# Kernel tuning notes

Hardware: AMD Instinct MI355X
Metric: run time of the kernel (lower is better)

Reference implementation:

```python
import jax, jax.numpy as jnp
import numpy as np

IN, H, OUT, B = 1024, 4096, 1, 4096


def setup_inputs() -> dict:
    key = jax.random.key(0)
    ks = jax.random.split(key, 20)
    sx = 1.0 / np.sqrt(IN)
    sh = 1.0 / np.sqrt(H)
    d = {
        "x": jax.random.normal(ks[0], (B, IN), jnp.float32),
        "hidden": jax.random.normal(ks[1], (B, H), jnp.float32),
        "cell": jax.random.normal(ks[2], (B, H), jnp.float32),
        # input projections (Linear(input_size, h_size)), weight [H, IN], bias [H]
        "Wx_i": jax.random.normal(ks[3], (H, IN), jnp.float32) * sx,
        "Wx_f": jax.random.normal(ks[4], (H, IN), jnp.float32) * sx,
        "Wx_o": jax.random.normal(ks[5], (H, IN), jnp.float32) * sx,
        "Wx_c": jax.random.normal(ks[6], (H, IN), jnp.float32) * sx,
        "bx_i": jax.random.normal(ks[7], (H,), jnp.float32) * sx,
        "bx_f": jax.random.normal(ks[8], (H,), jnp.float32) * sx,
        "bx_o": jax.random.normal(ks[9], (H,), jnp.float32) * sx,
        "bx_c": jax.random.normal(ks[10], (H,), jnp.float32) * sx,
        # hidden projections (Linear(h_size, h_size, bias=False)), weight [H, H]
        "Wh_i": jax.random.normal(ks[11], (H, H), jnp.float32) * sh,
        "Wh_f": jax.random.normal(ks[12], (H, H), jnp.float32) * sh,
        "Wh_o": jax.random.normal(ks[13], (H, H), jnp.float32) * sh,
        "Wh_c": jax.random.normal(ks[14], (H, H), jnp.float32) * sh,
        # output head Linear(h_size, out_size)
        "Wy": jax.random.normal(ks[15], (OUT, H), jnp.float32) * sh,
        "by": jax.random.normal(ks[16], (OUT,), jnp.float32) * sh,
    }
    return d


def reference(x, hidden, cell,
              Wx_i, Wx_f, Wx_o, Wx_c,
              bx_i, bx_f, bx_o, bx_c,
              Wh_i, Wh_f, Wh_o, Wh_c,
              Wy, by):
    # single LSTM step, batched over leading dim
    i = jax.nn.sigmoid(x @ Wx_i.T + bx_i + hidden @ Wh_i.T)
    f = jax.nn.sigmoid(x @ Wx_f.T + bx_f + hidden @ Wh_f.T)
    o = jax.nn.sigmoid(x @ Wx_o.T + bx_o + hidden @ Wh_o.T)
    c_til = jnp.tanh(x @ Wx_c.T + bx_c + hidden @ Wh_c.T)
    c_new = f * cell + i * c_til
    h_new = o * jnp.tanh(c_new)
    y_hat = h_new @ Wy.T + by  # [B, OUT]
    return y_hat
```

## Files before the change

kernel.cpp:

```cpp
#include <hip/hip_runtime.h>
#include <stdint.h>

#define IN_ 1024
#define H_  4096
#define B_  4096
#define K_  5120
#define NT_ 80

typedef short bf16x8 __attribute__((ext_vector_type(8)));
typedef float f32x4  __attribute__((ext_vector_type(4)));

__device__ __forceinline__ unsigned short f2bf(float x) {
    union { float f; uint32_t u; } v; v.f = x;
    return (unsigned short)((v.u + 0x7FFFu + ((v.u >> 16) & 1u)) >> 16);
}
__device__ __forceinline__ float bf2f(uint32_t u16) {
    union { uint32_t u; float f; } v; v.u = u16 << 16; return v.f;
}

__global__ __launch_bounds__(256) void cvt_cat(
    const float* __restrict__ s1, const float* __restrict__ s2,
    unsigned short* __restrict__ dst)
{
    int idx = blockIdx.x * 256 + threadIdx.x;
    int r = idx / (K_ / 4);
    int c = (idx % (K_ / 4)) * 4;
    float4 v;
    if (c < IN_) v = *(const float4*)(s1 + (size_t)r * IN_ + c);
    else         v = *(const float4*)(s2 + (size_t)r * H_ + (c - IN_));
    ushort4 o = { f2bf(v.x), f2bf(v.y), f2bf(v.z), f2bf(v.w) };
    *(ushort4*)(dst + (size_t)r * K_ + c) = o;
}

__device__ __forceinline__ int swz(int row) { return ((row >> 1) & 3) << 4; }

__global__ __launch_bounds__(512, 2) void gemm_gate8(
    const unsigned short* __restrict__ A,
    const unsigned short* __restrict__ W,
    const float* __restrict__ bias,
    unsigned short* __restrict__ P)
{
    __shared__ __align__(16) char ldsb[131072];

    const int tid  = threadIdx.x;
    const int wid  = tid >> 6;
    const int lane = tid & 63;

    const int wg = (blockIdx.x & 7) * 32 + (blockIdx.x >> 3);
    const int mt = wg & 15, nt = wg >> 4;
    const int bm = mt * 256, bn = nt * 256;

    const int wm = wid >> 2;
    const int wn = wid & 3;

    const int l15 = lane & 15;
    const int c0  = (lane >> 4) << 4;

    const int q0  = wid * 64 + lane;
    const int r0  = q0 >> 2;
    const int cb0 = ((q0 & 3) << 4) ^ swz(r0);
    const int r1  = r0 + 128;
    const int cb1 = ((q0 & 3) << 4) ^ swz(r1);

    f32x4 acc[8][4];
#pragma unroll
    for (int i = 0; i < 8; ++i)
#pragma unroll
        for (int j = 0; j < 4; ++j) acc[i][j] = (f32x4){0.f, 0.f, 0.f, 0.f};

    auto stage = [&](int isB, int ksel, int tau) {
        if (tau >= NT_) tau = NT_ - 2 + (tau & 1);
        const int kbase = tau * 64 + ksel * 32;
        const int chunk = (tau & 1) * 65536 + isB * 32768 + ksel * 16384;
        const unsigned short* src = isB ? W : A;
        const int gb = isB ? bn : bm;
        __builtin_amdgcn_global_load_lds(
            (const __attribute__((address_space(1))) void*)(src + (size_t)(gb + r0) * K_ + kbase + (cb0 >> 1)),
            (__attribute__((address_space(3))) void*)(ldsb + chunk + wid * 1024), 16, 0, 0);
        __builtin_amdgcn_global_load_lds(
            (const __attribute__((address_space(1))) void*)(src + (size_t)(gb + r1) * K_ + kbase + (cb1 >> 1)),
            (__attribute__((address_space(3))) void*)(ldsb + chunk + 8192 + wid * 1024), 16, 0, 0);
    };

    auto read_a = [&](bf16x8 dst[2][2], int kn) {
        const char* Ab = ldsb + (kn >> 2) * 65536;
        const int  nq  = kn & 3;
#pragma unroll
        for (int kh = 0; kh < 2; ++kh)
#pragma unroll
            for (int mi = 0; mi < 2; ++mi) {
                const int row = wm * 128 + nq * 32 + mi * 16 + l15;
                dst[kh][mi] = *(const bf16x8*)(Ab + kh * 16384 + row * 64 + (c0 ^ swz(row)));
            }
    };

    stage(0, 0, 0); stage(0, 1, 0); stage(1, 0, 0); stage(1, 1, 0);
    stage(0, 0, 1); stage(0, 1, 1); stage(1, 0, 1); stage(1, 1, 1);
    asm volatile("s_waitcnt vmcnt(8)" ::: "memory");
    __builtin_amdgcn_s_barrier();

    bf16x8 afrag[2][2][2];
    bf16x8 b[2][4];
    read_a(afrag[0], 0);

    for (int i = 0; i < NT_ / 2; ++i) {
        const int T0 = 2 * i;
#pragma unroll
        for (int k = 0; k < 8; ++k) {
            const int q   = k & 3;
            const int par = k & 1;
            const char* Bbase = ldsb + (k >> 2) * 65536 + 32768;

            if (q == 0) {
#pragma unroll
                for (int kh = 0; kh < 2; ++kh)
#pragma unroll
                    for (int ni = 0; ni < 4; ++ni) {
                        const int row = wn * 64 + ni * 16 + l15;
                        b[kh][ni] = *(const bf16x8*)(Bbase + kh * 16384 + row * 64 + (c0 ^ swz(row)));
                    }
            }
            if (q == 3) asm volatile("s_waitcnt vmcnt(4)" ::: "memory");
            __builtin_amdgcn_s_barrier();

            read_a(afrag[par ^ 1], (k + 1) & 7);
            __builtin_amdgcn_sched_barrier(0);

            __builtin_amdgcn_s_setprio(1);
#pragma unroll
            for (int mi = 0; mi < 2; ++mi)
#pragma unroll
                for (int ni = 0; ni < 4; ++ni)
                    acc[q * 2 + mi][ni] = __builtin_amdgcn_mfma_f32_16x16x32_bf16(
                        afrag[par][0][mi], b[0][ni], acc[q * 2 + mi][ni], 0, 0, 0);
#pragma unroll
            for (int mi = 0; mi < 2; ++mi)
#pragma unroll
                for (int ni = 0; ni < 4; ++ni)
                    acc[q * 2 + mi][ni] = __builtin_amdgcn_mfma_f32_16x16x32_bf16(
                        afrag[par][1][mi], b[1][ni], acc[q * 2 + mi][ni], 0, 0, 0);
            __builtin_amdgcn_s_setprio(0);

            if      (k == 0) stage(1, 0, T0 + 2);
            else if (k == 1) stage(1, 1, T0 + 2);
            else if (k == 2) stage(0, 0, T0 + 2);
            else if (k == 3) stage(0, 1, T0 + 2);
            else if (k == 4) stage(1, 0, T0 + 3);
            else if (k == 5) stage(1, 1, T0 + 3);
            else if (k == 6) stage(0, 0, T0 + 3);
            else             stage(0, 1, T0 + 3);
        }
    }

#pragma unroll
    for (int ni = 0; ni < 4; ++ni) {
        const int col = bn + wn * 64 + ni * 16 + l15;
        const float bv = bias[col];
#pragma unroll
        for (int mi = 0; mi < 8; ++mi) {
            const int row0 = bm + wm * 128 + mi * 16 + (lane >> 4) * 4;
#pragma unroll
            for (int r = 0; r < 4; ++r)
                P[(size_t)(row0 + r) * H_ + col] = f2bf(acc[mi][ni][r] + bv);
        }
    }
}

__global__ __launch_bounds__(256) void gates_gemv(
    const unsigned short* __restrict__ Pi, const unsigned short* __restrict__ Pf,
    const unsigned short* __restrict__ Po, const unsigned short* __restrict__ Pc,
    const float* __restrict__ cell, const float* __restrict__ Wy,
    const float* __restrict__ by, float* __restrict__ y)
{
    const int b = blockIdx.x;
    const int t = threadIdx.x;
    const size_t base = (size_t)b * H_;
    float part = 0.f;

#pragma unroll
    for (int j = 0; j < 4; ++j) {
        const int h = j * 1024 + t * 4;
        const uint2 ri = *(const uint2*)(Pi + base + h);
        const uint2 rf = *(const uint2*)(Pf + base + h);
        const uint2 ro = *(const uint2*)(Po + base + h);
        const uint2 rc = *(const uint2*)(Pc + base + h);
        const float4 cv = *(const float4*)(cell + base + h);
        const float4 wv = *(const float4*)(Wy + h);

        const uint32_t zi[4] = { ri.x & 0xffffu, ri.x >> 16, ri.y & 0xffffu, ri.y >> 16 };
        const uint32_t zf[4] = { rf.x & 0xffffu, rf.x >> 16, rf.y & 0xffffu, rf.y >> 16 };
        const uint32_t zo[4] = { ro.x & 0xffffu, ro.x >> 16, ro.y & 0xffffu, ro.y >> 16 };
        const uint32_t zc[4] = { rc.x & 0xffffu, rc.x >> 16, rc.y & 0xffffu, rc.y >> 16 };
        const float cc[4] = { cv.x, cv.y, cv.z, cv.w };
        const float ww[4] = { wv.x, wv.y, wv.z, wv.w };
#pragma unroll
        for (int e = 0; e < 4; ++e) {
            const float ig = 1.f / (1.f + __expf(-bf2f(zi[e])));
            const float fg = 1.f / (1.f + __expf(-bf2f(zf[e])));
            const float og = 1.f / (1.f + __expf(-bf2f(zo[e])));
            const float ct = tanhf(bf2f(zc[e]));
            const float cn = fg * cc[e] + ig * ct;
            const float hn = og * tanhf(cn);
            part += hn * ww[e];
        }
    }

#pragma unroll
    for (int off = 32; off > 0; off >>= 1) part += __shfl_down(part, off, 64);
    __shared__ float red[4];
    if ((t & 63) == 0) red[t >> 6] = part;
    __syncthreads();
    if (t == 0) y[b] = red[0] + red[1] + red[2] + red[3] + by[0];
}

extern "C" void kernel_launch(void* const* d_in, const int* in_sizes, int n_in,
                              void* d_out, int out_size, void* d_ws, size_t ws_size,
                              hipStream_t stream) {
    const float* x      = (const float*)d_in[0];
    const float* hidden = (const float*)d_in[1];
    const float* cell   = (const float*)d_in[2];
    const float* Wx[4]  = { (const float*)d_in[3], (const float*)d_in[4],
                            (const float*)d_in[5], (const float*)d_in[6] };
    const float* bx[4]  = { (const float*)d_in[7], (const float*)d_in[8],
                            (const float*)d_in[9], (const float*)d_in[10] };
    const float* Wh[4]  = { (const float*)d_in[11], (const float*)d_in[12],
                            (const float*)d_in[13], (const float*)d_in[14] };
    const float* Wy     = (const float*)d_in[15];
    const float* by     = (const float*)d_in[16];
    float* y = (float*)d_out;

    unsigned short* Ab = (unsigned short*)d_ws;
    unsigned short* Wb = Ab + (size_t)B_ * K_;
    unsigned short* Pg[4];
    {
        unsigned short* p0 = Wb + (size_t)H_ * K_;
        for (int g = 0; g < 4; ++g) Pg[g] = p0 + (size_t)g * B_ * H_;
    }

    const int cvt_grid = (B_ * (K_ / 4)) / 256;
    cvt_cat<<<cvt_grid, 256, 0, stream>>>(x, hidden, Ab);

    for (int g = 0; g < 4; ++g) {
        cvt_cat<<<cvt_grid, 256, 0, stream>>>(Wx[g], Wh[g], Wb);
        gemm_gate8<<<256, 512, 0, stream>>>(Ab, Wb, bx[g], Pg[g]);
    }

    gates_gemv<<<B_, 256, 0, stream>>>(Pg[0], Pg[1], Pg[2], Pg[3], cell, Wy, by, y);
}
```

Baseline: 714.2 us.

## Stagger warp LDS reads vs MFMA, rotate prefetch schedule, stage epilogue via LDS

Waves with wm==0 issue their next A-fragment LDS reads before the MFMA block, while the other waves issue them after it. This staggers LDS traffic against matrix work across waves. The global-to-LDS staging schedule is shifted by one slot so the prologue issues seven stages instead of eight, with the waitcnt adjusted to match. The epilogue now writes bf16 results into swizzled LDS and then stores them to global memory as coalesced 16-byte vectors, replacing the scattered 2-byte stores. In exchange it adds a full drain and barrier before the epilogue, and the reordered pipeline has to keep its waitcnt accounting correct.

```diff
diff --git a/kernel.cpp b/kernel.cpp
--- a/kernel.cpp
+++ b/kernel.cpp
@@ -94,13 +94,28 @@
             }
     };
 
-    stage(0, 0, 0); stage(0, 1, 0); stage(1, 0, 0); stage(1, 1, 0);
-    stage(0, 0, 1); stage(0, 1, 1); stage(1, 0, 1); stage(1, 1, 1);
-    asm volatile("s_waitcnt vmcnt(8)" ::: "memory");
-    __builtin_amdgcn_s_barrier();
-
     bf16x8 afrag[2][2][2];
     bf16x8 b[2][4];
+
+    auto mfma16 = [&](int q, int par) {
+#pragma unroll
+        for (int mi = 0; mi < 2; ++mi)
+#pragma unroll
+            for (int ni = 0; ni < 4; ++ni)
+                acc[q * 2 + mi][ni] = __builtin_amdgcn_mfma_f32_16x16x32_bf16(
+                    afrag[par][0][mi], b[0][ni], acc[q * 2 + mi][ni], 0, 0, 0);
+#pragma unroll
+        for (int mi = 0; mi < 2; ++mi)
+#pragma unroll
+            for (int ni = 0; ni < 4; ++ni)
+                acc[q * 2 + mi][ni] = __builtin_amdgcn_mfma_f32_16x16x32_bf16(
+                    afrag[par][1][mi], b[1][ni], acc[q * 2 + mi][ni], 0, 0, 0);
+    };
+
+    stage(0, 0, 0); stage(0, 1, 0); stage(1, 0, 0); stage(1, 1, 0);
+    stage(1, 0, 1); stage(1, 1, 1); stage(0, 0, 1);
+    asm volatile("s_waitcnt vmcnt(6)" ::: "memory");
+    __builtin_amdgcn_s_barrier();
     read_a(afrag[0], 0);
 
     for (int i = 0; i < NT_ / 2; ++i) {
@@ -123,46 +138,58 @@
             if (q == 3) asm volatile("s_waitcnt vmcnt(4)" ::: "memory");
             __builtin_amdgcn_s_barrier();
 
-            read_a(afrag[par ^ 1], (k + 1) & 7);
-            __builtin_amdgcn_sched_barrier(0);
-
-            __builtin_amdgcn_s_setprio(1);
-#pragma unroll
-            for (int mi = 0; mi < 2; ++mi)
-#pragma unroll
-                for (int ni = 0; ni < 4; ++ni)
-                    acc[q * 2 + mi][ni] = __builtin_amdgcn_mfma_f32_16x16x32_bf16(
-                        afrag[par][0][mi], b[0][ni], acc[q * 2 + mi][ni], 0, 0, 0);
-#pragma unroll
-            for (int mi = 0; mi < 2; ++mi)
-#pragma unroll
-                for (int ni = 0; ni < 4; ++ni)
-                    acc[q * 2 + mi][ni] = __builtin_amdgcn_mfma_f32_16x16x32_bf16(
-                        afrag[par][1][mi], b[1][ni], acc[q * 2 + mi][ni], 0, 0, 0);
-            __builtin_amdgcn_s_setprio(0);
-
-            if      (k == 0) stage(1, 0, T0 + 2);
-            else if (k == 1) stage(1, 1, T0 + 2);
-            else if (k == 2) stage(0, 0, T0 + 2);
-            else if (k == 3) stage(0, 1, T0 + 2);
-            else if (k == 4) stage(1, 0, T0 + 3);
-            else if (k == 5) stage(1, 1, T0 + 3);
-            else if (k == 6) stage(0, 0, T0 + 3);
-            else             stage(0, 1, T0 + 3);
+            if (wm == 0) {
+                read_a(afrag[par ^ 1], (k + 1) & 7);
+                __builtin_amdgcn_sched_barrier(0);
+                __builtin_amdgcn_s_setprio(1);
+                mfma16(q, par);
+                __builtin_amdgcn_s_setprio(0);
+            } else {
+                __builtin_amdgcn_s_setprio(1);
+                mfma16(q, par);
+                __builtin_amdgcn_s_setprio(0);
+                __builtin_amdgcn_sched_barrier(0);
+                read_a(afrag[par ^ 1], (k + 1) & 7);
+            }
+
+            if      (k == 0) stage(0, 1, T0 + 1);
+            else if (k == 1) stage(1, 0, T0 + 2);
+            else if (k == 2) stage(1, 1, T0 + 2);
+            else if (k == 3) stage(0, 0, T0 + 2);
+            else if (k == 4) stage(0, 1, T0 + 2);
+            else if (k == 5) stage(1, 0, T0 + 3);
+            else if (k == 6) stage(1, 1, T0 + 3);
+            else             stage(0, 0, T0 + 3);
         }
     }
 
+    asm volatile("s_waitcnt vmcnt(0)" ::: "memory");
+    __builtin_amdgcn_s_barrier();
+
 #pragma unroll
     for (int ni = 0; ni < 4; ++ni) {
-        const int col = bn + wn * 64 + ni * 16 + l15;
-        const float bv = bias[col];
+        const int col = wn * 64 + ni * 16 + l15;
+        const float bv = bias[bn + col];
 #pragma unroll
         for (int mi = 0; mi < 8; ++mi) {
-            const int row0 = bm + wm * 128 + mi * 16 + (lane >> 4) * 4;
-#pragma unroll
-            for (int r = 0; r < 4; ++r)
-                P[(size_t)(row0 + r) * H_ + col] = f2bf(acc[mi][ni][r] + bv);
+            const int row0 = wm * 128 + mi * 16 + (lane >> 4) * 4;
+#pragma unroll
+            for (int r = 0; r < 4; ++r) {
+                const int row = row0 + r;
+                const int byte = row * 512 + ((col * 2) ^ ((row & 7) << 4));
+                *(unsigned short*)(ldsb + byte) = f2bf(acc[mi][ni][r] + bv);
+            }
         }
+    }
+    __builtin_amdgcn_s_barrier();
+
+#pragma unroll
+    for (int c = 0; c < 16; ++c) {
+        const int idx = c * 512 + tid;
+        const int row = idx >> 5;
+        const int cb  = (idx & 31) * 16;
+        bf16x8 v = *(const bf16x8*)(ldsb + row * 512 + (cb ^ ((row & 7) << 4)));
+        *(bf16x8*)&P[(size_t)(bm + row) * H_ + bn + cb / 2] = v;
     }
 }
 
```

Result: slower. 1.334 ms (+86.7%).
